# Kernel tuning notes

Hardware: AMD Instinct MI355X
Metric: run time of the kernel (lower is better)

Reference implementation:

```python
import jax, jax.numpy as jnp
import numpy as np

N_NODES = 100000
NEG_SLOPE = 0.2


def setup_inputs() -> dict:
    key = jax.random.key(0)
    k1, k2, k3, k4, k5 = jax.random.split(key, 5)
    N, E, Fin, Fout = N_NODES, 3200000, 128, 128
    x = jax.random.normal(k1, (N, Fin), dtype=jnp.float32)
    edge_index = jax.random.randint(k2, (2, E), 0, N, dtype=jnp.int64)
    # xavier-uniform for lin weight (fan_in=Fin, fan_out=Fout)
    limit = float(np.sqrt(6.0 / (Fin + Fout)))
    W = jax.random.uniform(k3, (Fin, Fout), jnp.float32, -limit, limit)
    # PyG glorot init for attention vectors (fan ~ Fout)
    alim = float(np.sqrt(6.0 / (1 + Fout)))
    att_src = jax.random.uniform(k4, (Fout,), jnp.float32, -alim, alim)
    att_dst = jax.random.uniform(k5, (Fout,), jnp.float32, -alim, alim)
    bias = jnp.zeros((Fout,), jnp.float32)
    return {"x": x, "edge_index": edge_index, "W": W,
            "att_src": att_src, "att_dst": att_dst, "bias": bias}


def reference(x, edge_index, W, att_src, att_dst, bias):
    N = x.shape[0]
    src, dst = edge_index[0], edge_index[1]  # messages flow src -> dst
    h = x @ W                                # [N, Fout]
    a_src = h @ att_src                      # [N]
    a_dst = h @ att_dst                      # [N]
    e = a_src[src] + a_dst[dst]              # [E]
    e = jax.nn.leaky_relu(e, NEG_SLOPE)
    # segment softmax over incoming edges of each dst node
    e_max = jax.ops.segment_max(e, dst, num_segments=N)  # [N]
    e_max = jnp.where(jnp.isfinite(e_max), e_max, 0.0)
    e_exp = jnp.exp(e - e_max[dst])          # [E]
    denom = jax.ops.segment_sum(e_exp, dst, num_segments=N)  # [N]
    alpha = e_exp / (denom[dst] + 1e-16)     # [E]
    # scatter-add weighted neighbor features
    out = jax.ops.segment_sum(alpha[:, None] * h[src], dst, num_segments=N)
    out = out + bias
    return jax.nn.relu(out)
```

## Files before the change

### kernel.cpp

```cpp
#include <hip/hip_runtime.h>
#include <cstdint>
#include <cstddef>

#define NEG 0.2f
#define CAP 10752
#define FINE_CAP CAP

typedef __attribute__((ext_vector_type(8))) short short8;
typedef __attribute__((ext_vector_type(4))) float f32x4;

__device__ __forceinline__ unsigned short f2bf(float f) {
  unsigned u = __float_as_uint(f);
  unsigned r = (u + 0x7fffu + ((u >> 16) & 1u)) >> 16;
  return (unsigned short)r;
}

__global__ __launch_bounds__(512) void k_detect(const int* __restrict__ ei32,
                                                int* __restrict__ flag,
                                                int* __restrict__ cursor,
                                                const float* __restrict__ W,
                                                unsigned short* __restrict__ Wt) {
  int t = threadIdx.x;
  cursor[t] = t * CAP;
  if (t < 64) {
    int v = ei32[2 * t + 1];
    unsigned long long b = __ballot(v != 0);
    if (t == 0) flag[0] = (b == 0ULL) ? 1 : 0;
  }
#pragma unroll
  for (int i = 0; i < 8; ++i) {
    int idx = i * 512 + t;
    float4 v = ((const float4*)W)[idx];
    int k = idx >> 5;
    int c = (idx & 31) * 4;
    Wt[(c + 0) * 128 + k] = f2bf(v.x);
    Wt[(c + 1) * 128 + k] = f2bf(v.y);
    Wt[(c + 2) * 128 + k] = f2bf(v.z);
    Wt[(c + 3) * 128 + k] = f2bf(v.w);
  }
}

__device__ __forceinline__ int edge_val(const void* ei, long long idx, int is64) {
  return is64 ? (int)((const long long*)ei)[idx] : ((const int*)ei)[idx];
}

#define MS_CHUNK 4096
__global__ __launch_bounds__(256) void k_fused(
    const float* __restrict__ x, const unsigned short* __restrict__ Wt,
    const float* __restrict__ as_, const float* __restrict__ ad_,
    unsigned short* __restrict__ hb, float* __restrict__ a_s,
    float* __restrict__ a_d, int N,
    const void* __restrict__ ei, const int* __restrict__ flag,
    int* __restrict__ cursor, uint32_t* __restrict__ buck, int E, int nms) {
  __shared__ int hist[512];
  __shared__ int resv[512];
  int gid = blockIdx.x;
  int t = threadIdx.x;
  bool is_ms = ((gid % 3) == 0) && ((gid / 3) < nms);

  if (is_ms) {
    int bid = gid / 3;
    const int is64 = flag[0];
    for (int i = t; i < 512; i += 256) hist[i] = 0;
    __syncthreads();
    long long base = (long long)bid * MS_CHUNK;
    uint32_t rec[16];
    int bb[16], rk[16];
#pragma unroll
    for (int i = 0; i < 16; ++i) {
      long long idx = base + i * 256 + t;
      bb[i] = -1;
      if (idx < E) {
        int s = edge_val(ei, idx, is64);
        int d = edge_val(ei, (long long)E + idx, is64);
        bb[i] = d >> 8;
        rec[i] = ((uint32_t)(d & 255) << 17) | (uint32_t)s;
        rk[i] = atomicAdd(&hist[bb[i]], 1);
      }
    }
    __syncthreads();
    for (int b = t; b < 512; b += 256) {
      int c = hist[b];
      resv[b] = c ? atomicAdd(&cursor[b], c) : 0;
    }
    __syncthreads();
#pragma unroll
    for (int i = 0; i < 16; ++i) {
      if (bb[i] >= 0) buck[(size_t)resv[bb[i]] + rk[i]] = rec[i];
    }
    return;
  }

  int gemm_id = gid - min(gid / 3 + 1, nms);
  int lane = t & 63;
  int wv = t >> 6;
  int row0 = gemm_id * 64 + wv * 16;
  int r = lane & 15, o = lane >> 4;

  int arow = row0 + r;
  if (arow >= N) arow = N - 1;
  const float* xr = x + (size_t)arow * 128 + o * 8;
  short8 a[4];
#pragma unroll
  for (int kt = 0; kt < 4; ++kt) {
    float4 lo = *(const float4*)(xr + kt * 32);
    float4 hi = *(const float4*)(xr + kt * 32 + 4);
    short8 av;
    av[0] = (short)f2bf(lo.x); av[1] = (short)f2bf(lo.y);
    av[2] = (short)f2bf(lo.z); av[3] = (short)f2bf(lo.w);
    av[4] = (short)f2bf(hi.x); av[5] = (short)f2bf(hi.y);
    av[6] = (short)f2bf(hi.z); av[7] = (short)f2bf(hi.w);
    a[kt] = av;
  }

  float ats[8], atd[8];
#pragma unroll
  for (int ct = 0; ct < 8; ++ct) {
    ats[ct] = as_[ct * 16 + r];
    atd[ct] = ad_[ct * 16 + r];
  }

  f32x4 acc[8];
#pragma unroll
  for (int ct = 0; ct < 8; ++ct) acc[ct] = (f32x4){0.f, 0.f, 0.f, 0.f};
#pragma unroll
  for (int ct = 0; ct < 8; ++ct) {
    const unsigned short* wb = Wt + ((size_t)(ct * 16 + r)) * 128 + o * 8;
#pragma unroll
    for (int kt = 0; kt < 4; ++kt) {
      short8 b = *(const short8*)(wb + kt * 32);
      acc[ct] = __builtin_amdgcn_mfma_f32_16x16x32_bf16(a[kt], b, acc[ct], 0, 0, 0);
    }
  }

#pragma unroll
  for (int j = 0; j < 4; ++j) {
    int row = row0 + o * 4 + j;
    bool ok = row < N;
    float ps = 0.f, pd = 0.f;
#pragma unroll
    for (int ct = 0; ct < 8; ++ct) {
      float v = acc[ct][j];
      if (ok) hb[(size_t)row * 128 + ct * 16 + r] = f2bf(v);
      ps += v * ats[ct];
      pd += v * atd[ct];
    }
#pragma unroll
    for (int d = 1; d <= 8; d <<= 1) {
      ps += __shfl_xor(ps, d);
      pd += __shfl_xor(pd, d);
    }
    if (ok && r == 0) { a_s[row] = ps; a_d[row] = pd; }
  }
}

__global__ __launch_bounds__(1024) void k_fine(const int* __restrict__ cursor,
                                               const uint32_t* __restrict__ buck,
                                               int* __restrict__ offsets,
                                               uint32_t* __restrict__ fsr,
                                               int N, int E) {
  __shared__ int hist[256];
  __shared__ int cur[256];
  __shared__ int wsum8[8];
  __shared__ int wsum[4];
  __shared__ int b0_sh;
  __shared__ uint32_t stage[FINE_CAP];
  int b = blockIdx.x;
  int t = threadIdx.x;
  int lane = t & 63;
  int cnt = cursor[b] - b * CAP;
  const uint32_t* bk = buck + (size_t)b * CAP;
  int node = (b << 8) + (t & 255);

  int sv = 0, sincl = 0, sw8 = t >> 6;
  if (t < 512) {
    sv = cursor[t] - t * CAP;
    sincl = sv;
#pragma unroll
    for (int d = 1; d < 64; d <<= 1) {
      int o = __shfl_up(sincl, d);
      if (lane >= d) sincl += o;
    }
    if (lane == 63) wsum8[sw8] = sincl;
  }
  if (t < 256) hist[t] = 0;
  __syncthreads();
  if (t < 512) {
    int woff = 0;
    for (int i = 0; i < sw8; ++i) woff += wsum8[i];
    int excl = woff + sincl - sv;
    if (t == b) b0_sh = excl;
  }
  __syncthreads();
  int b0 = b0_sh;

  for (int i = t; i < cnt; i += 1024) atomicAdd(&hist[bk[i] >> 17], 1);
  __syncthreads();
  int v = 0, incl = 0;
  int w4 = t >> 6;
  if (t < 256) {
    v = hist[t];
    incl = v;
#pragma unroll
    for (int d = 1; d < 64; d <<= 1) {
      int o = __shfl_up(incl, d);
      if (lane >= d) incl += o;
    }
    if (lane == 63) wsum[w4] = incl;
  }
  __syncthreads();
  if (t < 256) {
    int woff = 0;
    for (int i = 0; i < w4; ++i) woff += wsum[i];
    int excl = woff + incl - v;
    cur[t] = excl;
    if (node < N) offsets[node] = b0 + excl;
  }
  if (b == 0 && t == 0) offsets[N] = E;
  __syncthreads();
  for (int i = t; i < cnt; i += 1024) {
    uint32_t r = bk[i];
    int pos = atomicAdd(&cur[r >> 17], 1);
    stage[pos] = r;
  }
  __syncthreads();
  for (int i = t; i < cnt; i += 1024) fsr[b0 + i] = stage[i];
}

#define AGG_LOAD(K, JJ)                                                   \
  {                                                                       \
    int e_ = ((JJ) * 4 + g) & 63;                                         \
    int ss_ = __shfl(s_l, e_);                                            \
    float ww_ = __shfl(w_l, e_);                                          \
    w##K = ((JJ) < iters) ? ww_ : 0.f;                                    \
    u##K = *(const uint4*)&hb[(size_t)ss_ * 128 + l16 * 8];               \
  }

#define AGG_FMA(K)                                                        \
  {                                                                       \
    acc[0] += w##K * __uint_as_float(u##K.x << 16);                       \
    acc[1] += w##K * __uint_as_float(u##K.x & 0xffff0000u);               \
    acc[2] += w##K * __uint_as_float(u##K.y << 16);                       \
    acc[3] += w##K * __uint_as_float(u##K.y & 0xffff0000u);               \
    acc[4] += w##K * __uint_as_float(u##K.z << 16);                       \
    acc[5] += w##K * __uint_as_float(u##K.z & 0xffff0000u);               \
    acc[6] += w##K * __uint_as_float(u##K.w << 16);                       \
    acc[7] += w##K * __uint_as_float(u##K.w & 0xffff0000u);               \
  }

__global__ __launch_bounds__(256) void k_agg(const int* __restrict__ offs,
                                             const uint32_t* __restrict__ fsr,
                                             const float* __restrict__ a_s,
                                             const float* __restrict__ a_d,
                                             const unsigned short* __restrict__ hb,
                                             const float* __restrict__ bias,
                                             float* __restrict__ out, int N) {
  int lane = threadIdx.x & 63;
  int n = blockIdx.x * 4 + (threadIdx.x >> 6);
  if (n >= N) return;
  int g = lane >> 4;
  int l16 = lane & 15;
  float acc[8] = {};
  float sum = 0.f;
  int s0 = offs[n], s1 = offs[n + 1];
  float adn = a_d[n];

  for (int base = s0; base < s1; base += 64) {
    int idx = base + lane;
    int s_l = 0;
    float w_l = 0.f;
    if (idx < s1) {
      uint32_t r = fsr[idx];
      s_l = (int)(r & 0x1ffffu);
      float e = a_s[s_l] + adn;
      e = (e > 0.f) ? e : NEG * e;
      w_l = __expf(e);
    }
    sum += w_l;
    int cnt = min(64, s1 - base);
    int iters = (cnt + 3) >> 2;
    uint4 u0, u1, u2, u3, u4;
    float w0, w1, w2, w3, w4;
    AGG_LOAD(0, 0) AGG_LOAD(1, 1) AGG_LOAD(2, 2)
    AGG_LOAD(3, 3) AGG_LOAD(4, 4)
    int j = 0;
    for (; j + 5 < iters; j += 5) {
      AGG_FMA(0) AGG_LOAD(0, j + 5)
      AGG_FMA(1) AGG_LOAD(1, j + 6)
      AGG_FMA(2) AGG_LOAD(2, j + 7)
      AGG_FMA(3) AGG_LOAD(3, j + 8)
      AGG_FMA(4) AGG_LOAD(4, j + 9)
    }
    AGG_FMA(0) AGG_FMA(1) AGG_FMA(2) AGG_FMA(3) AGG_FMA(4)
  }
#pragma unroll
  for (int d = 1; d <= 32; d <<= 1) sum += __shfl_xor(sum, d);
#pragma unroll
  for (int d = 16; d <= 32; d <<= 1) {
#pragma unroll
    for (int i = 0; i < 8; ++i) acc[i] += __shfl_xor(acc[i], d);
  }
  float inv = 1.0f / (sum + 1e-16f);
  if (lane < 32) {
    int half = g & 1;
    int f = l16 * 8 + half * 4;
    float4 bv = *(const float4*)&bias[f];
    float4 o;
    o.x = fmaxf(acc[half * 4 + 0] * inv + bv.x, 0.f);
    o.y = fmaxf(acc[half * 4 + 1] * inv + bv.y, 0.f);
    o.z = fmaxf(acc[half * 4 + 2] * inv + bv.z, 0.f);
    o.w = fmaxf(acc[half * 4 + 3] * inv + bv.w, 0.f);
    *(float4*)&out[(size_t)n * 128 + f] = o;
  }
}

extern "C" void kernel_launch(void* const* d_in, const int* in_sizes, int n_in,
                              void* d_out, int out_size, void* d_ws, size_t ws_size,
                              hipStream_t stream) {
  const float* x = (const float*)d_in[0];
  const void* ei = d_in[1];
  const float* W = (const float*)d_in[2];
  const float* att_s = (const float*)d_in[3];
  const float* att_d = (const float*)d_in[4];
  const float* bias = (const float*)d_in[5];
  float* out = (float*)d_out;

  const int N = in_sizes[0] / 128;
  const int E = in_sizes[1] / 2;
  const int NB = (N + 255) >> 8;

  uint8_t* ws = (uint8_t*)d_ws;
  size_t off = 0;
  auto alloc = [&](size_t bytes) -> void* {
    void* p = ws + off;
    off = (off + bytes + 511) & ~(size_t)511;
    return p;
  };
  int* flag = (int*)alloc(4);
  int* bcur = (int*)alloc(512 * 4);
  unsigned short* Wt = (unsigned short*)alloc(128 * 128 * 2);
  int* offsets = (int*)alloc((size_t)(N + 1) * 4);
  uint32_t* fsr = (uint32_t*)alloc((size_t)E * 4);
  unsigned short* hb = (unsigned short*)alloc((size_t)N * 128 * 2);
  float* a_s = (float*)alloc((size_t)N * 4);
  float* a_d = (float*)alloc((size_t)N * 4);
  uint32_t* buck = (uint32_t*)d_out;
  (void)ws_size; (void)n_in; (void)out_size;

  const int ngemm = (N + 63) / 64;
  const int nms = (E + MS_CHUNK - 1) / MS_CHUNK;
  int grid = ngemm + nms;
  if (grid < 3 * nms - 2) grid = 3 * nms - 2;

  k_detect<<<1, 512, 0, stream>>>((const int*)ei, flag, bcur, W, Wt);
  k_fused<<<grid, 256, 0, stream>>>(x, Wt, att_s, att_d, hb, a_s, a_d, N,
                                    ei, flag, bcur, buck, E, nms);
  k_fine<<<NB, 1024, 0, stream>>>(bcur, buck, offsets, fsr, N, E);
  k_agg<<<(N + 3) / 4, 256, 0, stream>>>(offsets, fsr, a_s, a_d, hb, bias, out, N);
}
```

Baseline: 190.9 us.

## Stage bucketed edges in shared memory to coalesce bucket scatter writes

The bucketing blocks now split each 4096-edge chunk into two 2048-edge batches. For each batch they compute a block-local exclusive scan of the per-bucket histogram and stage the edges in LDS sorted by bucket. Consecutive threads then write to contiguous positions within each bucket's reserved range, replacing random per-thread global scatter writes. This adds shared memory (16KB of staging), extra barriers, and a second histogram/atomic round per chunk, which may lower occupancy for the co-resident GEMM blocks.

```diff
diff --git a/kernel.cpp b/kernel.cpp
--- a/kernel.cpp
+++ b/kernel.cpp
@@ -53,7 +53,10 @@
     const void* __restrict__ ei, const int* __restrict__ flag,
     int* __restrict__ cursor, uint32_t* __restrict__ buck, int E, int nms) {
   __shared__ int hist[512];
+  __shared__ int excl_s[512];
   __shared__ int resv[512];
+  __shared__ int wsum_ms[4];
+  __shared__ int2 stage_ms[2048];
   int gid = blockIdx.x;
   int t = threadIdx.x;
   bool is_ms = ((gid % 3) == 0) && ((gid / 3) < nms);
@@ -61,32 +64,58 @@
   if (is_ms) {
     int bid = gid / 3;
     const int is64 = flag[0];
-    for (int i = t; i < 512; i += 256) hist[i] = 0;
-    __syncthreads();
-    long long base = (long long)bid * MS_CHUNK;
-    uint32_t rec[16];
-    int bb[16], rk[16];
-#pragma unroll
-    for (int i = 0; i < 16; ++i) {
-      long long idx = base + i * 256 + t;
-      bb[i] = -1;
-      if (idx < E) {
-        int s = edge_val(ei, idx, is64);
-        int d = edge_val(ei, (long long)E + idx, is64);
-        bb[i] = d >> 8;
-        rec[i] = ((uint32_t)(d & 255) << 17) | (uint32_t)s;
-        rk[i] = atomicAdd(&hist[bb[i]], 1);
+#pragma unroll
+    for (int batch = 0; batch < 2; ++batch) {
+      long long bb0 = (long long)bid * MS_CHUNK + batch * 2048;
+      long long rem = (long long)E - bb0;
+      if (rem <= 0) break;
+      int valid = (rem < 2048) ? (int)rem : 2048;
+      for (int i = t; i < 512; i += 256) hist[i] = 0;
+      __syncthreads();
+      int d_[8], s_[8], rk[8];
+#pragma unroll
+      for (int i = 0; i < 8; ++i) {
+        int idx = i * 256 + t;
+        d_[i] = -1;
+        if (idx < valid) {
+          s_[i] = edge_val(ei, bb0 + idx, is64);
+          d_[i] = edge_val(ei, (long long)E + bb0 + idx, is64);
+          rk[i] = atomicAdd(&hist[d_[i] >> 8], 1);
+        }
       }
-    }
-    __syncthreads();
-    for (int b = t; b < 512; b += 256) {
-      int c = hist[b];
-      resv[b] = c ? atomicAdd(&cursor[b], c) : 0;
-    }
-    __syncthreads();
-#pragma unroll
-    for (int i = 0; i < 16; ++i) {
-      if (bb[i] >= 0) buck[(size_t)resv[bb[i]] + rk[i]] = rec[i];
+      __syncthreads();
+      int h0 = hist[2 * t], h1 = hist[2 * t + 1];
+      int pv = h0 + h1;
+      int lane_ = t & 63, wv_ = t >> 6;
+      int incl_ = pv;
+#pragma unroll
+      for (int dd = 1; dd < 64; dd <<= 1) {
+        int o = __shfl_up(incl_, dd);
+        if (lane_ >= dd) incl_ += o;
+      }
+      if (lane_ == 63) wsum_ms[wv_] = incl_;
+      __syncthreads();
+      int woff = 0;
+      for (int i = 0; i < wv_; ++i) woff += wsum_ms[i];
+      int excl_pair = woff + incl_ - pv;
+      excl_s[2 * t] = excl_pair;
+      excl_s[2 * t + 1] = excl_pair + h0;
+      resv[2 * t] = h0 ? atomicAdd(&cursor[2 * t], h0) : 0;
+      resv[2 * t + 1] = h1 ? atomicAdd(&cursor[2 * t + 1], h1) : 0;
+      __syncthreads();
+#pragma unroll
+      for (int i = 0; i < 8; ++i) {
+        if (d_[i] >= 0)
+          stage_ms[excl_s[d_[i] >> 8] + rk[i]] = make_int2(d_[i], s_[i]);
+      }
+      __syncthreads();
+      for (int i = t; i < valid; i += 256) {
+        int2 e = stage_ms[i];
+        int b = e.x >> 8;
+        buck[(size_t)resv[b] + (i - excl_s[b])] =
+            ((uint32_t)(e.x & 255) << 17) | (uint32_t)e.y;
+      }
+      __syncthreads();
     }
     return;
   }
```

After: 212.4 us. 11.3% more time.
